# Kernel tuning notes

Measured on AMD Instinct MI355X. Metric: run time of the kernel, lower is better.

The kernel has to match this reference:

```python
import jax, jax.numpy as jnp
import numpy as np

WINDOW = 8
HEADS = 12
HEAD_DIM = 64
DISP = WINDOW // 2  # cyclic shift displacement
WS2 = WINDOW * WINDOW


def _rel_indices():
    idx = np.array([[x, y] for x in range(WINDOW) for y in range(WINDOW)])  # (ws2,2)
    rel = idx[None, :, :] - idx[:, None, :] + (WINDOW - 1)  # (ws2,ws2,2)
    return rel


def _create_mask(upper_lower, left_right):
    m = np.zeros((WS2, WS2), dtype=np.float32)
    d = DISP
    if upper_lower:
        m[-d * WINDOW:, :-d * WINDOW] = -np.inf
        m[:-d * WINDOW, -d * WINDOW:] = -np.inf
    if left_right:
        m4 = m.reshape(WINDOW, WINDOW, WINDOW, WINDOW)
        m4[:, -d:, :, :-d] = -np.inf
        m4[:, :-d, :, -d:] = -np.inf
        m = m4.reshape(WS2, WS2)
    return m


def _window_masks(n_h, n_w):
    # per-window additive mask, (n_h*n_w, ws2, ws2)
    ul = _create_mask(True, False)
    lr = _create_mask(False, True)
    masks = np.zeros((n_h * n_w, WS2, WS2), dtype=np.float32)
    masks[-n_w:] += ul                 # last row of windows
    masks[n_w - 1::n_w] += lr          # last column of windows
    return masks


def _to_windows(x, n_h, n_w):
    # x: (b, c, h, w) -> (b, heads, n_windows, ws2, head_dim)
    b = x.shape[0]
    x = x.reshape(b, HEADS, HEAD_DIM, n_h, WINDOW, n_w, WINDOW)
    x = x.transpose(0, 1, 3, 5, 4, 6, 2)
    return x.reshape(b, HEADS, n_h * n_w, WS2, HEAD_DIM)


def setup_inputs() -> dict:
    key = jax.random.key(0)
    ks = jax.random.split(key, 8)
    B, H, W, C = 8, 64, 64, HEADS * HEAD_DIM
    return {
        "q_feat": jax.random.normal(ks[0], (B, H * W, C), dtype=jnp.float32),
        "k_feat": jax.random.normal(ks[1], (B, H * W, C), dtype=jnp.float32),
        "v_feat": jax.random.normal(ks[2], (B, H * W, C), dtype=jnp.float32),
        "Wq": jax.random.normal(ks[3], (HEAD_DIM, HEAD_DIM), dtype=jnp.float32) * 0.05,
        "Wk": jax.random.normal(ks[4], (HEAD_DIM, HEAD_DIM), dtype=jnp.float32) * 0.05,
        "Wv": jax.random.normal(ks[5], (HEAD_DIM, HEAD_DIM), dtype=jnp.float32) * 0.05,
        "Wlin": jax.random.normal(ks[6], (HEAD_DIM, HEAD_DIM), dtype=jnp.float32) * 0.05,
        "pe": jax.random.normal(ks[7], (2 * WINDOW - 1, 2 * WINDOW - 1), dtype=jnp.float32),
        "h": 64,
        "w": 64,
    }


def reference(q_feat, k_feat, v_feat, Wq, Wk, Wv, Wlin, pe, h, w):
    b, hw, c = q_feat.shape
    n_h, n_w = h // WINDOW, w // WINDOW
    rel = _rel_indices()
    win_mask = jnp.asarray(_window_masks(n_h, n_w))  # (nwin, ws2, ws2)

    def to_img(f):  # (b, h*w, c) -> (b, c, h, w)
        return f.transpose(0, 2, 1).reshape(b, c, h, w)

    qi = jnp.roll(to_img(q_feat), (-DISP, -DISP), axis=(2, 3))
    ki = jnp.roll(to_img(k_feat), (-DISP, -DISP), axis=(2, 3))
    vi = jnp.roll(to_img(v_feat), (-DISP, -DISP), axis=(2, 3))

    qw = _to_windows(qi, n_h, n_w)  # (b, heads, nwin, ws2, hd)
    kw = _to_windows(ki, n_h, n_w)
    vw = _to_windows(vi, n_h, n_w)

    q = jnp.einsum('bhnsd,ed->bhnse', qw, Wq)
    k = jnp.einsum('bhnsd,ed->bhnse', kw, Wk)
    v = jnp.einsum('bhnsd,ed->bhnse', vw, Wv)

    qk = jnp.einsum('bhnqd,bhnkd->bhnqk', q, k) / np.sqrt(HEAD_DIM).astype(np.float32)
    bias = pe[rel[:, :, 0], rel[:, :, 1]]  # (ws2, ws2)
    qk = qk + bias[None, None, None] + win_mask[None, None]

    attn = jax.nn.softmax(qk, axis=-1)
    out = jnp.einsum('bhnqk,bhnkd->bhnqd', attn, v)
    out = jnp.einsum('bhnsd,ed->bhnse', out, Wlin)

    # windows back to image: (b,heads,nwin,ws2,hd) -> (b,c,h,w)
    out = out.transpose(0, 1, 4, 2, 3).reshape(b, c, n_h, n_w, WINDOW, WINDOW)
    out = out.transpose(0, 1, 2, 4, 3, 5).reshape(b, c, h, w)
    out = jnp.roll(out, (DISP, DISP), axis=(2, 3))
    out = out.reshape(b, c, h * w).transpose(0, 2, 1)  # (b, h*w, c)
    return out, attn
```

## Files before the change

### kernel.cpp

```cpp
#include <hip/hip_runtime.h>
#include <hip/hip_bf16.h>

typedef __bf16 bf16x8 __attribute__((ext_vector_type(8)));
typedef float f32x4 __attribute__((ext_vector_type(4)));
typedef float f32x8 __attribute__((ext_vector_type(8)));
typedef unsigned short u16x8 __attribute__((ext_vector_type(8)));

#define MFMA16(a, b, c) __builtin_amdgcn_mfma_f32_16x16x32_bf16((a), (b), (c), 0, 0, 0)

static __device__ __forceinline__ unsigned short f2b(float f) {
    union { float f; unsigned int u; } v; v.f = f;
    unsigned int r = v.u + 0x7FFFu + ((v.u >> 16) & 1u);
    return (unsigned short)(r >> 16);
}
static __device__ __forceinline__ float b2f(unsigned short s) {
    union { unsigned int u; float f; } v; v.u = ((unsigned int)s) << 16;
    return v.f;
}
static __device__ __forceinline__ bf16x8 cvtv(f32x8 v) {
    bf16x8 r;
    #pragma unroll
    for (int i = 0; i < 8; ++i) r[i] = (__bf16)v[i];
    return r;
}

__global__ __launch_bounds__(256) void precompute_mn(
    const float* __restrict__ Wq, const float* __restrict__ Wk,
    const float* __restrict__ Wv, const float* __restrict__ Wl,
    unsigned short* __restrict__ ws)
{
    __shared__ float A[4096], B[4096];
    const int bid = blockIdx.x;
    const int which = bid >> 2;
    const int rq = bid & 3;
    const int tid = threadIdx.x;
    for (int i = tid; i < 4096; i += 256) {
        A[i] = which ? Wl[i] : Wq[i];
        B[i] = which ? Wv[i] : Wk[i];
    }
    __syncthreads();
    const int row = rq * 16 + (tid >> 4);
    const int c0  = tid & 15;
    float acc[4] = {0, 0, 0, 0};
    if (which == 0) {
        for (int e = 0; e < 64; ++e) {
            const float s = A[e * 64 + row];
            #pragma unroll
            for (int i = 0; i < 4; ++i) acc[i] += s * B[e * 64 + c0 + 16 * i];
        }
    } else {
        for (int c = 0; c < 64; ++c) {
            const float s = A[row * 64 + c];
            #pragma unroll
            for (int i = 0; i < 4; ++i) acc[i] += s * B[c * 64 + c0 + 16 * i];
        }
    }
    #pragma unroll
    for (int i = 0; i < 4; ++i)
        ws[which * 4096 + row * 64 + c0 + 16 * i] = f2b(acc[i]);
}

#define PITCH 68

__global__ __launch_bounds__(512) void swca_fused(
    const float* __restrict__ qf,
    const float* __restrict__ kf,
    const float* __restrict__ vf,
    const unsigned short* __restrict__ Mw,
    const unsigned short* __restrict__ Nw,
    const float* __restrict__ pe,
    float* __restrict__ out,
    float* __restrict__ attn,
    int nblk2)
{
    __shared__ unsigned short kmS[2][64][PITCH];
    __shared__ unsigned short vnT[2][64][PITCH];
    __shared__ unsigned short As[2][64][PITCH];

    int bid = blockIdx.x;
    const int nper = nblk2 >> 3;
    const int task2 = (bid & 7) * nper + (bid >> 3);

    const int tid = threadIdx.x;
    const int h2  = tid >> 8;
    int task = task2 * 2 + h2;

    const int head = task % 12; task /= 12;
    const int win  = task & 63;
    const int b    = task >> 6;
    const int wy = win >> 3, wx = win & 7;

    const int tt   = tid & 255;
    const int wid  = tt >> 6;
    const int lane = tt & 63;
    const int lg   = lane >> 4;
    const int lc   = lane & 15;
    const int srow = wid * 16 + lc;

    const int sy = srow >> 3, sx = srow & 7;
    const int gy = (wy * 8 + sy + 4) & 63;
    const int gx = (wx * 8 + sx + 4) & 63;
    const long rowbase = ((long)b * 4096 + gy * 64 + gx) * 768 + head * 64;

    auto ld8 = [](const unsigned short* p) -> bf16x8 {
        return *reinterpret_cast<const bf16x8*>(p);
    };

    bf16x8 kb0 = cvtv(*reinterpret_cast<const f32x8*>(kf + rowbase + lg * 8));
    bf16x8 kb1 = cvtv(*reinterpret_cast<const f32x8*>(kf + rowbase + 32 + lg * 8));
    bf16x8 vb0 = cvtv(*reinterpret_cast<const f32x8*>(vf + rowbase + lg * 8));
    bf16x8 vb1 = cvtv(*reinterpret_cast<const f32x8*>(vf + rowbase + 32 + lg * 8));
    bf16x8 qa0 = cvtv(*reinterpret_cast<const f32x8*>(qf + rowbase + lg * 8));
    bf16x8 qa1 = cvtv(*reinterpret_cast<const f32x8*>(qf + rowbase + 32 + lg * 8));

    {
        f32x4 acc[4] = {};
        #pragma unroll
        for (int t = 0; t < 4; ++t) {
            acc[t] = MFMA16(kb0, ld8(Mw + (t * 16 + lc) * 64 + lg * 8), acc[t]);
            acc[t] = MFMA16(kb1, ld8(Mw + (t * 16 + lc) * 64 + 32 + lg * 8), acc[t]);
        }
        #pragma unroll
        for (int t = 0; t < 4; ++t)
            #pragma unroll
            for (int j = 0; j < 4; ++j)
                kmS[h2][wid * 16 + lg * 4 + j][t * 16 + lc] = f2b(acc[t][j]);
    }
    {
        f32x4 acc[4] = {};
        #pragma unroll
        for (int t = 0; t < 4; ++t) {
            acc[t] = MFMA16(vb0, ld8(Nw + (t * 16 + lc) * 64 + lg * 8), acc[t]);
            acc[t] = MFMA16(vb1, ld8(Nw + (t * 16 + lc) * 64 + 32 + lg * 8), acc[t]);
        }
        #pragma unroll
        for (int t = 0; t < 4; ++t)
            #pragma unroll
            for (int j = 0; j < 4; ++j)
                vnT[h2][t * 16 + lc][wid * 16 + lg * 4 + j] = f2b(acc[t][j]);
    }
    __syncthreads();

    f32x4 accS[4] = {};
    {
        #pragma unroll
        for (int t = 0; t < 4; ++t) {
            accS[t] = MFMA16(qa0, ld8(&kmS[h2][t * 16 + lc][lg * 8]), accS[t]);
            accS[t] = MFMA16(qa1, ld8(&kmS[h2][t * 16 + lc][32 + lg * 8]), accS[t]);
        }
    }
    const int r0 = wid * 16 + lg * 4;
    {
        float sv[4][4];
        #pragma unroll
        for (int t = 0; t < 4; ++t) {
            const int c = t * 16 + lc, ky = c >> 3, kx = c & 7;
            #pragma unroll
            for (int j = 0; j < 4; ++j) {
                const int r = r0 + j, qy = r >> 3, qx = r & 7;
                const float biasv = pe[(ky - qy + 7) * 15 + (kx - qx + 7)];
                const bool msk = ((wy == 7) && (((qy ^ ky) & 4) != 0)) ||
                                 ((wx == 7) && (((qx ^ kx) & 4) != 0));
                sv[t][j] = msk ? -__builtin_inff() : accS[t][j] * 0.125f + biasv;
            }
        }
        #pragma unroll
        for (int j = 0; j < 4; ++j) {
            float mx = fmaxf(fmaxf(sv[0][j], sv[1][j]), fmaxf(sv[2][j], sv[3][j]));
            mx = fmaxf(mx, __shfl_xor(mx, 1));
            mx = fmaxf(mx, __shfl_xor(mx, 2));
            mx = fmaxf(mx, __shfl_xor(mx, 4));
            mx = fmaxf(mx, __shfl_xor(mx, 8));
            const float e0 = __expf(sv[0][j] - mx);
            const float e1 = __expf(sv[1][j] - mx);
            const float e2 = __expf(sv[2][j] - mx);
            const float e3 = __expf(sv[3][j] - mx);
            float sm = (e0 + e1) + (e2 + e3);
            sm += __shfl_xor(sm, 1);
            sm += __shfl_xor(sm, 2);
            sm += __shfl_xor(sm, 4);
            sm += __shfl_xor(sm, 8);
            const float inv = 1.0f / sm;
            As[h2][r0 + j][0 * 16 + lc] = f2b(e0 * inv);
            As[h2][r0 + j][1 * 16 + lc] = f2b(e1 * inv);
            As[h2][r0 + j][2 * 16 + lc] = f2b(e2 * inv);
            As[h2][r0 + j][3 * 16 + lc] = f2b(e3 * inv);
        }
    }

    {
        const int lr = wid * 16 + (lane >> 2);
        const int c0 = (lane & 3) * 16;
        u16x8 p0 = *reinterpret_cast<const u16x8*>(&As[h2][lr][c0]);
        u16x8 p1 = *reinterpret_cast<const u16x8*>(&As[h2][lr][c0 + 8]);
        const long abase = ((((long)b * 12 + head) * 64 + win) * 64 + lr) * 64 + c0;
        f32x4 o0, o1, o2, o3;
        #pragma unroll
        for (int i = 0; i < 4; ++i) { o0[i] = b2f(p0[i]); o1[i] = b2f(p0[4 + i]); }
        #pragma unroll
        for (int i = 0; i < 4; ++i) { o2[i] = b2f(p1[i]); o3[i] = b2f(p1[4 + i]); }
        *reinterpret_cast<f32x4*>(attn + abase)      = o0;
        *reinterpret_cast<f32x4*>(attn + abase + 4)  = o1;
        *reinterpret_cast<f32x4*>(attn + abase + 8)  = o2;
        *reinterpret_cast<f32x4*>(attn + abase + 12) = o3;
    }

    {
        bf16x8 a0 = ld8(&As[h2][srow][lg * 8]);
        bf16x8 a1 = ld8(&As[h2][srow][32 + lg * 8]);
        f32x4 acc[4] = {};
        #pragma unroll
        for (int t = 0; t < 4; ++t) {
            acc[t] = MFMA16(a0, ld8(&vnT[h2][t * 16 + lc][lg * 8]), acc[t]);
            acc[t] = MFMA16(a1, ld8(&vnT[h2][t * 16 + lc][32 + lg * 8]), acc[t]);
        }
        #pragma unroll
        for (int j = 0; j < 4; ++j) {
            const int r = r0 + j, ry = r >> 3, rx = r & 7;
            const int oy = (wy * 8 + ry + 4) & 63;
            const int ox = (wx * 8 + rx + 4) & 63;
            const long obase = ((long)b * 4096 + oy * 64 + ox) * 768 + head * 64;
            #pragma unroll
            for (int t = 0; t < 4; ++t)
                out[obase + t * 16 + lc] = acc[t][j];
        }
    }
}

extern "C" void kernel_launch(void* const* d_in, const int* in_sizes, int n_in,
                              void* d_out, int out_size, void* d_ws, size_t ws_size,
                              hipStream_t stream) {
    const float* qf = (const float*)d_in[0];
    const float* kf = (const float*)d_in[1];
    const float* vf = (const float*)d_in[2];
    const float* Wq = (const float*)d_in[3];
    const float* Wk = (const float*)d_in[4];
    const float* Wv = (const float*)d_in[5];
    const float* Wl = (const float*)d_in[6];
    const float* pe = (const float*)d_in[7];

    const int B = in_sizes[0] / (4096 * 768);
    float* outp = (float*)d_out;
    float* attnp = outp + (size_t)B * 4096 * 768;
    unsigned short* ws = (unsigned short*)d_ws;

    precompute_mn<<<8, 256, 0, stream>>>(Wq, Wk, Wv, Wl, ws);

    const int nblk2 = B * 768 / 2;
    swca_fused<<<nblk2, 512, 0, stream>>>(qf, kf, vf, ws, ws + 4096, pe,
                                          outp, attnp, nblk2);
}
```

Baseline: 143.0 us.

## Make blocks persistent over six tasks and prefetch next task's inputs

Each block now loops over six (head, window, batch) tasks instead of one, so the grid shrinks sixfold. The next task's q/k/v rows are loaded into registers while the current task computes attention, overlapping global-memory latency with MFMA and softmax work. This costs more registers per thread and an extra barrier per iteration. The block-to-task mapping hardcodes 64 groups per XCD slice, which assumes B=8, and launch bounds now request 4 blocks per CU.

```diff
diff --git a/kernel.cpp b/kernel.cpp
--- a/kernel.cpp
+++ b/kernel.cpp
@@ -61,8 +61,9 @@
 }
 
 #define PITCH 68
-
-__global__ __launch_bounds__(512) void swca_fused(
+#define NT 6
+
+__global__ __launch_bounds__(512, 4) void swca_fused(
     const float* __restrict__ qf,
     const float* __restrict__ kf,
     const float* __restrict__ vf,
@@ -70,160 +71,185 @@
     const unsigned short* __restrict__ Nw,
     const float* __restrict__ pe,
     float* __restrict__ out,
-    float* __restrict__ attn,
-    int nblk2)
+    float* __restrict__ attn)
 {
     __shared__ unsigned short kmS[2][64][PITCH];
     __shared__ unsigned short vnT[2][64][PITCH];
     __shared__ unsigned short As[2][64][PITCH];
 
-    int bid = blockIdx.x;
-    const int nper = nblk2 >> 3;
-    const int task2 = (bid & 7) * nper + (bid >> 3);
+    const int bid = blockIdx.x;
+    const int g = (bid & 7) * 64 + (bid >> 3);
 
     const int tid = threadIdx.x;
     const int h2  = tid >> 8;
-    int task = task2 * 2 + h2;
-
-    const int head = task % 12; task /= 12;
-    const int win  = task & 63;
-    const int b    = task >> 6;
-    const int wy = win >> 3, wx = win & 7;
-
     const int tt   = tid & 255;
     const int wid  = tt >> 6;
     const int lane = tt & 63;
     const int lg   = lane >> 4;
     const int lc   = lane & 15;
     const int srow = wid * 16 + lc;
-
     const int sy = srow >> 3, sx = srow & 7;
-    const int gy = (wy * 8 + sy + 4) & 63;
-    const int gx = (wx * 8 + sx + 4) & 63;
-    const long rowbase = ((long)b * 4096 + gy * 64 + gx) * 768 + head * 64;
+    const int r0 = wid * 16 + lg * 4;
 
     auto ld8 = [](const unsigned short* p) -> bf16x8 {
         return *reinterpret_cast<const bf16x8*>(p);
     };
-
-    bf16x8 kb0 = cvtv(*reinterpret_cast<const f32x8*>(kf + rowbase + lg * 8));
-    bf16x8 kb1 = cvtv(*reinterpret_cast<const f32x8*>(kf + rowbase + 32 + lg * 8));
-    bf16x8 vb0 = cvtv(*reinterpret_cast<const f32x8*>(vf + rowbase + lg * 8));
-    bf16x8 vb1 = cvtv(*reinterpret_cast<const f32x8*>(vf + rowbase + 32 + lg * 8));
-    bf16x8 qa0 = cvtv(*reinterpret_cast<const f32x8*>(qf + rowbase + lg * 8));
-    bf16x8 qa1 = cvtv(*reinterpret_cast<const f32x8*>(qf + rowbase + 32 + lg * 8));
-
-    {
-        f32x4 acc[4] = {};
-        #pragma unroll
-        for (int t = 0; t < 4; ++t) {
-            acc[t] = MFMA16(kb0, ld8(Mw + (t * 16 + lc) * 64 + lg * 8), acc[t]);
-            acc[t] = MFMA16(kb1, ld8(Mw + (t * 16 + lc) * 64 + 32 + lg * 8), acc[t]);
-        }
-        #pragma unroll
-        for (int t = 0; t < 4; ++t)
-            #pragma unroll
-            for (int j = 0; j < 4; ++j)
-                kmS[h2][wid * 16 + lg * 4 + j][t * 16 + lc] = f2b(acc[t][j]);
-    }
-    {
-        f32x4 acc[4] = {};
-        #pragma unroll
-        for (int t = 0; t < 4; ++t) {
-            acc[t] = MFMA16(vb0, ld8(Nw + (t * 16 + lc) * 64 + lg * 8), acc[t]);
-            acc[t] = MFMA16(vb1, ld8(Nw + (t * 16 + lc) * 64 + 32 + lg * 8), acc[t]);
-        }
-        #pragma unroll
-        for (int t = 0; t < 4; ++t)
-            #pragma unroll
-            for (int j = 0; j < 4; ++j)
-                vnT[h2][t * 16 + lc][wid * 16 + lg * 4 + j] = f2b(acc[t][j]);
-    }
-    __syncthreads();
-
-    f32x4 accS[4] = {};
-    {
-        #pragma unroll
-        for (int t = 0; t < 4; ++t) {
-            accS[t] = MFMA16(qa0, ld8(&kmS[h2][t * 16 + lc][lg * 8]), accS[t]);
-            accS[t] = MFMA16(qa1, ld8(&kmS[h2][t * 16 + lc][32 + lg * 8]), accS[t]);
-        }
-    }
-    const int r0 = wid * 16 + lg * 4;
-    {
-        float sv[4][4];
-        #pragma unroll
-        for (int t = 0; t < 4; ++t) {
-            const int c = t * 16 + lc, ky = c >> 3, kx = c & 7;
+    auto rbase = [&](int hd, int wn, int bb) -> long {
+        const int wy = wn >> 3, wx = wn & 7;
+        const int gy = (wy * 8 + sy + 4) & 63;
+        const int gx = (wx * 8 + sx + 4) & 63;
+        return ((long)bb * 4096 + gy * 64 + gx) * 768 + hd * 64;
+    };
+
+    int task = g * 12 + h2;
+    int headC = task % 12;
+    int winC  = (task / 12) & 63;
+    int bC    = (task / 12) >> 6;
+
+    long rb = rbase(headC, winC, bC);
+    f32x8 ck0 = *reinterpret_cast<const f32x8*>(kf + rb + lg * 8);
+    f32x8 ck1 = *reinterpret_cast<const f32x8*>(kf + rb + 32 + lg * 8);
+    f32x8 cv0 = *reinterpret_cast<const f32x8*>(vf + rb + lg * 8);
+    f32x8 cv1 = *reinterpret_cast<const f32x8*>(vf + rb + 32 + lg * 8);
+    f32x8 cq0 = *reinterpret_cast<const f32x8*>(qf + rb + lg * 8);
+    f32x8 cq1 = *reinterpret_cast<const f32x8*>(qf + rb + 32 + lg * 8);
+
+    for (int it = 0; it < NT; ++it) {
+        {
+            bf16x8 kb0 = cvtv(ck0), kb1 = cvtv(ck1);
+            f32x4 acc[4] = {};
+            #pragma unroll
+            for (int t = 0; t < 4; ++t) {
+                acc[t] = MFMA16(kb0, ld8(Mw + (t * 16 + lc) * 64 + lg * 8), acc[t]);
+                acc[t] = MFMA16(kb1, ld8(Mw + (t * 16 + lc) * 64 + 32 + lg * 8), acc[t]);
+            }
+            #pragma unroll
+            for (int t = 0; t < 4; ++t)
+                #pragma unroll
+                for (int j = 0; j < 4; ++j)
+                    kmS[h2][wid * 16 + lg * 4 + j][t * 16 + lc] = f2b(acc[t][j]);
+        }
+        {
+            bf16x8 vb0 = cvtv(cv0), vb1 = cvtv(cv1);
+            f32x4 acc[4] = {};
+            #pragma unroll
+            for (int t = 0; t < 4; ++t) {
+                acc[t] = MFMA16(vb0, ld8(Nw + (t * 16 + lc) * 64 + lg * 8), acc[t]);
+                acc[t] = MFMA16(vb1, ld8(Nw + (t * 16 + lc) * 64 + 32 + lg * 8), acc[t]);
+            }
+            #pragma unroll
+            for (int t = 0; t < 4; ++t)
+                #pragma unroll
+                for (int j = 0; j < 4; ++j)
+                    vnT[h2][t * 16 + lc][wid * 16 + lg * 4 + j] = f2b(acc[t][j]);
+        }
+        __syncthreads();
+
+        f32x8 nk0 = {}, nk1 = {}, nv0 = {}, nv1 = {}, nq0 = {}, nq1 = {};
+        int headN = 0, winN = 0, bN = 0;
+        if (it + 1 < NT) {
+            const int tn = task + 2;
+            headN = tn % 12; winN = (tn / 12) & 63; bN = (tn / 12) >> 6;
+            const long rbn = rbase(headN, winN, bN);
+            nk0 = *reinterpret_cast<const f32x8*>(kf + rbn + lg * 8);
+            nk1 = *reinterpret_cast<const f32x8*>(kf + rbn + 32 + lg * 8);
+            nv0 = *reinterpret_cast<const f32x8*>(vf + rbn + lg * 8);
+            nv1 = *reinterpret_cast<const f32x8*>(vf + rbn + 32 + lg * 8);
+            nq0 = *reinterpret_cast<const f32x8*>(qf + rbn + lg * 8);
+            nq1 = *reinterpret_cast<const f32x8*>(qf + rbn + 32 + lg * 8);
+        }
+        const int wy = winC >> 3, wx = winC & 7;
+
+        f32x4 accS[4] = {};
+        {
+            bf16x8 qa0 = cvtv(cq0), qa1 = cvtv(cq1);
+            #pragma unroll
+            for (int t = 0; t < 4; ++t) {
+                accS[t] = MFMA16(qa0, ld8(&kmS[h2][t * 16 + lc][lg * 8]), accS[t]);
+                accS[t] = MFMA16(qa1, ld8(&kmS[h2][t * 16 + lc][32 + lg * 8]), accS[t]);
+            }
+        }
+        {
+            float sv[4][4];
+            #pragma unroll
+            for (int t = 0; t < 4; ++t) {
+                const int c = t * 16 + lc, ky = c >> 3, kx = c & 7;
+                #pragma unroll
+                for (int j = 0; j < 4; ++j) {
+                    const int r = r0 + j, qy = r >> 3, qx = r & 7;
+                    const float biasv = pe[(ky - qy + 7) * 15 + (kx - qx + 7)];
+                    const bool msk = ((wy == 7) && (((qy ^ ky) & 4) != 0)) ||
+                                     ((wx == 7) && (((qx ^ kx) & 4) != 0));
+                    sv[t][j] = msk ? -__builtin_inff() : accS[t][j] * 0.125f + biasv;
+                }
+            }
             #pragma unroll
             for (int j = 0; j < 4; ++j) {
-                const int r = r0 + j, qy = r >> 3, qx = r & 7;
-                const float biasv = pe[(ky - qy + 7) * 15 + (kx - qx + 7)];
-                const bool msk = ((wy == 7) && (((qy ^ ky) & 4) != 0)) ||
-                                 ((wx == 7) && (((qx ^ kx) & 4) != 0));
-                sv[t][j] = msk ? -__builtin_inff() : accS[t][j] * 0.125f + biasv;
-            }
-        }
-        #pragma unroll
-        for (int j = 0; j < 4; ++j) {
-            float mx = fmaxf(fmaxf(sv[0][j], sv[1][j]), fmaxf(sv[2][j], sv[3][j]));
-            mx = fmaxf(mx, __shfl_xor(mx, 1));
-            mx = fmaxf(mx, __shfl_xor(mx, 2));
-            mx = fmaxf(mx, __shfl_xor(mx, 4));
-            mx = fmaxf(mx, __shfl_xor(mx, 8));
-            const float e0 = __expf(sv[0][j] - mx);
-            const float e1 = __expf(sv[1][j] - mx);
-            const float e2 = __expf(sv[2][j] - mx);
-            const float e3 = __expf(sv[3][j] - mx);
-            float sm = (e0 + e1) + (e2 + e3);
-            sm += __shfl_xor(sm, 1);
-            sm += __shfl_xor(sm, 2);
-            sm += __shfl_xor(sm, 4);
-            sm += __shfl_xor(sm, 8);
-            const float inv = 1.0f / sm;
-            As[h2][r0 + j][0 * 16 + lc] = f2b(e0 * inv);
-            As[h2][r0 + j][1 * 16 + lc] = f2b(e1 * inv);
-            As[h2][r0 + j][2 * 16 + lc] = f2b(e2 * inv);
-            As[h2][r0 + j][3 * 16 + lc] = f2b(e3 * inv);
-        }
-    }
-
-    {
-        const int lr = wid * 16 + (lane >> 2);
-        const int c0 = (lane & 3) * 16;
-        u16x8 p0 = *reinterpret_cast<const u16x8*>(&As[h2][lr][c0]);
-        u16x8 p1 = *reinterpret_cast<const u16x8*>(&As[h2][lr][c0 + 8]);
-        const long abase = ((((long)b * 12 + head) * 64 + win) * 64 + lr) * 64 + c0;
-        f32x4 o0, o1, o2, o3;
-        #pragma unroll
-        for (int i = 0; i < 4; ++i) { o0[i] = b2f(p0[i]); o1[i] = b2f(p0[4 + i]); }
-        #pragma unroll
-        for (int i = 0; i < 4; ++i) { o2[i] = b2f(p1[i]); o3[i] = b2f(p1[4 + i]); }
-        *reinterpret_cast<f32x4*>(attn + abase)      = o0;
-        *reinterpret_cast<f32x4*>(attn + abase + 4)  = o1;
-        *reinterpret_cast<f32x4*>(attn + abase + 8)  = o2;
-        *reinterpret_cast<f32x4*>(attn + abase + 12) = o3;
-    }
-
-    {
-        bf16x8 a0 = ld8(&As[h2][srow][lg * 8]);
-        bf16x8 a1 = ld8(&As[h2][srow][32 + lg * 8]);
-        f32x4 acc[4] = {};
-        #pragma unroll
-        for (int t = 0; t < 4; ++t) {
-            acc[t] = MFMA16(a0, ld8(&vnT[h2][t * 16 + lc][lg * 8]), acc[t]);
-            acc[t] = MFMA16(a1, ld8(&vnT[h2][t * 16 + lc][32 + lg * 8]), acc[t]);
-        }
-        #pragma unroll
-        for (int j = 0; j < 4; ++j) {
-            const int r = r0 + j, ry = r >> 3, rx = r & 7;
-            const int oy = (wy * 8 + ry + 4) & 63;
-            const int ox = (wx * 8 + rx + 4) & 63;
-            const long obase = ((long)b * 4096 + oy * 64 + ox) * 768 + head * 64;
-            #pragma unroll
-            for (int t = 0; t < 4; ++t)
-                out[obase + t * 16 + lc] = acc[t][j];
-        }
+                float mx = fmaxf(fmaxf(sv[0][j], sv[1][j]), fmaxf(sv[2][j], sv[3][j]));
+                mx = fmaxf(mx, __shfl_xor(mx, 1));
+                mx = fmaxf(mx, __shfl_xor(mx, 2));
+                mx = fmaxf(mx, __shfl_xor(mx, 4));
+                mx = fmaxf(mx, __shfl_xor(mx, 8));
+                const float e0 = __expf(sv[0][j] - mx);
+                const float e1 = __expf(sv[1][j] - mx);
+                const float e2 = __expf(sv[2][j] - mx);
+                const float e3 = __expf(sv[3][j] - mx);
+                float sm = (e0 + e1) + (e2 + e3);
+                sm += __shfl_xor(sm, 1);
+                sm += __shfl_xor(sm, 2);
+                sm += __shfl_xor(sm, 4);
+                sm += __shfl_xor(sm, 8);
+                const float inv = 1.0f / sm;
+                As[h2][r0 + j][0 * 16 + lc] = f2b(e0 * inv);
+                As[h2][r0 + j][1 * 16 + lc] = f2b(e1 * inv);
+                As[h2][r0 + j][2 * 16 + lc] = f2b(e2 * inv);
+                As[h2][r0 + j][3 * 16 + lc] = f2b(e3 * inv);
+            }
+        }
+
+        {
+            const int lr = wid * 16 + (lane >> 2);
+            const int c0 = (lane & 3) * 16;
+            u16x8 p0 = *reinterpret_cast<const u16x8*>(&As[h2][lr][c0]);
+            u16x8 p1 = *reinterpret_cast<const u16x8*>(&As[h2][lr][c0 + 8]);
+            const long abase = ((((long)bC * 12 + headC) * 64 + winC) * 64 + lr) * 64 + c0;
+            f32x4 o0, o1, o2, o3;
+            #pragma unroll
+            for (int i = 0; i < 4; ++i) { o0[i] = b2f(p0[i]); o1[i] = b2f(p0[4 + i]); }
+            #pragma unroll
+            for (int i = 0; i < 4; ++i) { o2[i] = b2f(p1[i]); o3[i] = b2f(p1[4 + i]); }
+            *reinterpret_cast<f32x4*>(attn + abase)      = o0;
+            *reinterpret_cast<f32x4*>(attn + abase + 4)  = o1;
+            *reinterpret_cast<f32x4*>(attn + abase + 8)  = o2;
+            *reinterpret_cast<f32x4*>(attn + abase + 12) = o3;
+        }
+
+        {
+            bf16x8 a0 = ld8(&As[h2][srow][lg * 8]);
+            bf16x8 a1 = ld8(&As[h2][srow][32 + lg * 8]);
+            f32x4 acc[4] = {};
+            #pragma unroll
+            for (int t = 0; t < 4; ++t) {
+                acc[t] = MFMA16(a0, ld8(&vnT[h2][t * 16 + lc][lg * 8]), acc[t]);
+                acc[t] = MFMA16(a1, ld8(&vnT[h2][t * 16 + lc][32 + lg * 8]), acc[t]);
+            }
+            #pragma unroll
+            for (int j = 0; j < 4; ++j) {
+                const int r = r0 + j, ry = r >> 3, rx = r & 7;
+                const int oy = (wy * 8 + ry + 4) & 63;
+                const int ox = (wx * 8 + rx + 4) & 63;
+                const long obase = ((long)bC * 4096 + oy * 64 + ox) * 768 + headC * 64;
+                #pragma unroll
+                for (int t = 0; t < 4; ++t)
+                    out[obase + t * 16 + lc] = acc[t][j];
+            }
+        }
+
+        __syncthreads();
+
+        ck0 = nk0; ck1 = nk1; cv0 = nv0; cv1 = nv1; cq0 = nq0; cq1 = nq1;
+        headC = headN; winC = winN; bC = bN;
+        task += 2;
     }
 }
 
@@ -246,7 +272,7 @@
 
     precompute_mn<<<8, 256, 0, stream>>>(Wq, Wk, Wv, Wl, ws);
 
-    const int nblk2 = B * 768 / 2;
-    swca_fused<<<nblk2, 512, 0, stream>>>(qf, kf, vf, ws, ws + 4096, pe,
-                                          outp, attnp, nblk2);
-}
+    const int nblk = B * 768 / (2 * NT);
+    swca_fused<<<nblk, 512, 0, stream>>>(qf, kf, vf, ws, ws + 4096, pe,
+                                         outp, attnp);
+}
```

Result: slower. 244.8 us (+71.1%).
